# Optimization experiments

Hardware: AMD Instinct MI355X
Metric: run time of the kernel (lower is better)

Reference implementation:

```python
import jax, jax.numpy as jnp
import numpy as np

N = 100000  # nodes
E = 1600000  # edges
N_IN, N_H = 256, 128


def _norms(edge_src, edge_dst):
    ones = jnp.ones((E,), dtype=jnp.float32)
    out_deg = jax.ops.segment_sum(ones, edge_src, num_segments=N)
    in_deg = jax.ops.segment_sum(ones, edge_dst, num_segments=N)
    # DGL clamps degrees to >= 1 for norm='both'
    norm_src = jnp.clip(out_deg, 1.0, None) ** -0.5  # [N]
    norm_dst = jnp.clip(in_deg, 1.0, None) ** -0.5   # [N]
    return norm_src, norm_dst


def _graph_conv(h, W, b, edge_src, edge_dst, norm_src, norm_dst):
    # symmetric norm: D_out^{-1/2} A D_in^{-1/2}; W applied pre-aggregation
    h = h * norm_src[:, None]          # [N, d_in]
    h = h @ W                          # [N, d_out]
    msg = h[edge_src]                  # [E, d_out] gather
    agg = jax.ops.segment_sum(msg, edge_dst, num_segments=N)  # scatter-add
    agg = agg * norm_dst[:, None]
    return jax.nn.relu(agg + b)


def setup_inputs() -> dict:
    key = jax.random.key(0)
    ks = jax.random.split(key, 7)
    feat = jax.random.normal(ks[0], (1, N, N_IN), dtype=jnp.float32)
    edge_src = jax.random.randint(ks[1], (E,), 0, N, dtype=jnp.int32)
    edge_dst = jax.random.randint(ks[2], (E,), 0, N, dtype=jnp.int32)
    # Glorot-uniform weights as in DGL GraphConv reset_parameters
    lim1 = (6.0 / (N_IN + N_H)) ** 0.5
    lim2 = (6.0 / (N_H + N_H)) ** 0.5
    W1 = jax.random.uniform(ks[3], (N_IN, N_H), jnp.float32, -lim1, lim1)
    b1 = jnp.zeros((N_H,), dtype=jnp.float32)
    W2 = jax.random.uniform(ks[4], (N_H, N_H), jnp.float32, -lim2, lim2)
    b2 = jnp.zeros((N_H,), dtype=jnp.float32)
    return {"feat": feat, "W1": W1, "b1": b1, "W2": W2, "b2": b2,
            "edge_src": edge_src, "edge_dst": edge_dst}


def reference(feat, W1, b1, W2, b2, edge_src, edge_dst):
    h = feat.squeeze(0)  # [N, n_in]
    norm_src, norm_dst = _norms(edge_src, edge_dst)
    h = _graph_conv(h, W1, b1, edge_src, edge_dst, norm_src, norm_dst)
    h = _graph_conv(h, W2, b2, edge_src, edge_dst, norm_src, norm_dst)
    return h
```

## Files before the change

### kernel.cpp

```cpp
#include <hip/hip_runtime.h>
#include <hip/hip_bf16.h>

#define N_NODES 100000
#define N_EDGES 1600000
#define NBUCK 391
#define NBLK 256
#define CHUNK (N_EDGES / NBLK)
#define MATP (NBUCK * NBLK)

typedef float f32x4 __attribute__((ext_vector_type(4)));
typedef _Float16 f16x8 __attribute__((ext_vector_type(8)));

__device__ __forceinline__ void wt_elem(const float* __restrict__ W,
                                        _Float16* __restrict__ WTf,
                                        int K, int i) {
    int col = i / K, k = i - col * K;
    WTf[i] = (_Float16)W[(size_t)k * 128 + col];
}

__global__ __launch_bounds__(256) void fused_setup(
    const int* __restrict__ esrc, const int* __restrict__ edst,
    int* __restrict__ cnt_mat,
    const float* __restrict__ W1, _Float16* __restrict__ WT1f,
    const float* __restrict__ W2, _Float16* __restrict__ WT2f)
{
    __shared__ int hd[NBUCK], hs[NBUCK];
    const int b = blockIdx.x, t = threadIdx.x;
    if (b < NBLK) {
        for (int i = t; i < NBUCK; i += 256) { hd[i] = 0; hs[i] = 0; }
        __syncthreads();
        const int e1 = (b + 1) * CHUNK;
        for (int e = b * CHUNK + t; e < e1; e += 256) {
            atomicAdd(&hd[edst[e] >> 8], 1);
            atomicAdd(&hs[esrc[e] >> 8], 1);
        }
        __syncthreads();
        for (int i = t; i < NBUCK; i += 256) {
            cnt_mat[i * NBLK + b] = hd[i];
            cnt_mat[MATP + i * NBLK + b] = hs[i];
        }
    } else {
        int i = (b - NBLK) * 256 + t;
        if (i < 128 * 256) {
            wt_elem(W1, WT1f, 256, i);
        } else {
            int j = i - 128 * 256;
            wt_elem(W2, WT2f, 128, j);
        }
    }
}

__global__ __launch_bounds__(1024) void scan_blocks(const int* __restrict__ counts,
                                                    int* __restrict__ out,
                                                    int* __restrict__ partials, int n) {
    __shared__ int tmp[1024];
    int i = blockIdx.x * 1024 + threadIdx.x;
    int v = (i < n) ? counts[i] : 0;
    tmp[threadIdx.x] = v;
    __syncthreads();
    for (int off = 1; off < 1024; off <<= 1) {
        int t = (threadIdx.x >= (unsigned)off) ? tmp[threadIdx.x - off] : 0;
        __syncthreads();
        tmp[threadIdx.x] += t;
        __syncthreads();
    }
    if (i < n) out[i] = tmp[threadIdx.x] - v;
    if (threadIdx.x == 1023) partials[blockIdx.x] = tmp[1023];
}

__global__ __launch_bounds__(256) void scan_partials(int* __restrict__ partials, int nb) {
    __shared__ int tmp[256];
    int t = threadIdx.x;
    int v = (t < nb) ? partials[t] : 0;
    tmp[t] = v;
    __syncthreads();
    for (int off = 1; off < 256; off <<= 1) {
        int u = (t >= off) ? tmp[t - off] : 0;
        __syncthreads();
        tmp[t] += u;
        __syncthreads();
    }
    if (t < nb) partials[t] = tmp[t] - v;
}

__device__ __forceinline__ int sm_at(const int* __restrict__ scan_mat,
                                     const int* __restrict__ partials, int i) {
    return scan_mat[i] + partials[i >> 10];
}

__global__ __launch_bounds__(256) void bucket_scatter(const int* __restrict__ esrc,
                                                      const int* __restrict__ edst,
                                                      const int* __restrict__ scan_mat,
                                                      const int* __restrict__ partials,
                                                      unsigned int* __restrict__ tmp,
                                                      unsigned char* __restrict__ tmp2) {
    __shared__ int cd[NBUCK], cs[NBUCK];
    const int b = blockIdx.x, t = threadIdx.x;
    for (int i = t; i < NBUCK; i += 256) {
        cd[i] = sm_at(scan_mat, partials, i * NBLK + b);
        cs[i] = sm_at(scan_mat, partials, MATP + i * NBLK + b) - N_EDGES;
    }
    __syncthreads();
    const int e1 = (b + 1) * CHUNK;
    for (int e = b * CHUNK + t; e < e1; e += 256) {
        int s = esrc[e], d = edst[e];
        int pd = atomicAdd(&cd[d >> 8], 1);
        tmp[pd] = ((unsigned int)(d & 255) << 17) | (unsigned int)s;
        int ps = atomicAdd(&cs[s >> 8], 1);
        tmp2[ps] = (unsigned char)(s & 255);
    }
}

__global__ __launch_bounds__(256) void finalize_fused(
    const unsigned int* __restrict__ tmp,
    const unsigned char* __restrict__ tmp2,
    const int* __restrict__ scan_mat,
    const int* __restrict__ partials,
    int* __restrict__ rowptr,
    int* __restrict__ csr_src,
    float* __restrict__ ndst,
    float* __restrict__ nsrc)
{
    __shared__ int hist[256];
    __shared__ int scn[256];
    __shared__ int cur[256];
    const int bb = blockIdx.x, t = threadIdx.x;
    if (bb < NBUCK) {
        const int b = bb;
        const int beg = sm_at(scan_mat, partials, b * 256);
        const int end = sm_at(scan_mat, partials, (b + 1) * 256);
        hist[t] = 0;
        __syncthreads();
        for (int j = beg + t; j < end; j += 256)
            atomicAdd(&hist[tmp[j] >> 17], 1);
        __syncthreads();
        int v = hist[t];
        scn[t] = v;
        __syncthreads();
        for (int off = 1; off < 256; off <<= 1) {
            int u = (t >= off) ? scn[t - off] : 0;
            __syncthreads();
            scn[t] += u;
            __syncthreads();
        }
        int excl = scn[t] - v;
        int node = b * 256 + t;
        if (node <= N_NODES) rowptr[node] = beg + excl;
        if (node < N_NODES) ndst[node] = rsqrtf(fmaxf((float)v, 1.0f));
        cur[t] = beg + excl;
        __syncthreads();
        for (int j = beg + t; j < end; j += 256) {
            unsigned int x = tmp[j];
            int pos = atomicAdd(&cur[x >> 17], 1);
            csr_src[pos] = (int)(x & 0x1FFFFu);
        }
    } else {
        const int b = bb - NBUCK;
        const int beg = sm_at(scan_mat, partials, MATP + b * 256) - N_EDGES;
        const int end = (b < NBUCK - 1)
                          ? sm_at(scan_mat, partials, MATP + (b + 1) * 256) - N_EDGES
                          : N_EDGES;
        hist[t] = 0;
        __syncthreads();
        for (int j = beg + t; j < end; j += 256)
            atomicAdd(&hist[tmp2[j]], 1);
        __syncthreads();
        int node = b * 256 + t;
        if (node < N_NODES) nsrc[node] = rsqrtf(fmaxf((float)hist[t], 1.0f));
    }
}

template<int K, int ATERMS, typename AT>
__global__ __launch_bounds__(256) void gemm_mfma(
    const AT* __restrict__ A,
    const _Float16* __restrict__ WTf,
    const float* __restrict__ rowscale,
    _Float16* __restrict__ C16,
    int M)
{
    constexpr int ASTR = 520;
    constexpr int BSTR = 1032;
    __shared__ _Float16 Ah[8 * ASTR];
    __shared__ _Float16 Al[ATERMS == 2 ? 8 * ASTR : 8];
    __shared__ _Float16 Bf[8 * BSTR];

    const int tid = threadIdx.x;
    const int bm = blockIdx.x * 64;
    const int lane = tid & 63;
    const int wid = tid >> 6;
    const int wm = wid >> 1;
    const int wn = wid & 1;
    const int lr = lane & 15;
    const int lg = lane >> 4;

    f32x4 acc[2][4];
    #pragma unroll
    for (int i = 0; i < 2; ++i)
        #pragma unroll
        for (int j = 0; j < 4; ++j)
            acc[i][j] = (f32x4){0.f, 0.f, 0.f, 0.f};

    float avreg[2][8];
    f16x8 areg16[2];
    f16x8 bv[4];

    auto load_tile = [&](int k0) {
        #pragma unroll
        for (int i = 0; i < 2; ++i) {
            int lin = tid + i * 256;
            int row = lin >> 3;
            int s8  = lin & 7;
            int rg  = bm + row;
            if (rg < M) {
                const AT* ap = &A[(size_t)rg * K + k0 + s8 * 8];
                if constexpr (sizeof(AT) == 4) {
                    float4 v0 = *reinterpret_cast<const float4*>(ap);
                    float4 v1 = *reinterpret_cast<const float4*>(ap + 4);
                    avreg[i][0] = v0.x; avreg[i][1] = v0.y; avreg[i][2] = v0.z; avreg[i][3] = v0.w;
                    avreg[i][4] = v1.x; avreg[i][5] = v1.y; avreg[i][6] = v1.z; avreg[i][7] = v1.w;
                } else {
                    areg16[i] = *reinterpret_cast<const f16x8*>(ap);
                }
            } else {
                if constexpr (sizeof(AT) == 4) {
                    #pragma unroll
                    for (int j = 0; j < 8; ++j) avreg[i][j] = 0.f;
                } else {
                    #pragma unroll
                    for (int j = 0; j < 8; ++j) areg16[i][j] = (_Float16)0.f;
                }
            }
        }
        #pragma unroll
        for (int i = 0; i < 4; ++i) {
            int lin = tid + i * 256;
            int col = lin >> 3;
            int s8  = lin & 7;
            bv[i] = *reinterpret_cast<const f16x8*>(&WTf[(size_t)col * K + k0 + s8 * 8]);
        }
    };

    load_tile(0);

    for (int k0 = 0; k0 < K; k0 += 64) {
        {
            #pragma unroll
            for (int i = 0; i < 2; ++i) {
                int lin = tid + i * 256;
                int row = lin >> 3;
                int s8  = lin & 7;
                int off = s8 * ASTR + row * 8;
                if constexpr (sizeof(AT) == 4) {
                    f16x8 vh, vl;
                    #pragma unroll
                    for (int j = 0; j < 8; ++j) {
                        _Float16 h = (_Float16)avreg[i][j];
                        vh[j] = h;
                        vl[j] = (_Float16)(avreg[i][j] - (float)h);
                    }
                    *reinterpret_cast<f16x8*>(&Ah[off]) = vh;
                    if constexpr (ATERMS == 2)
                        *reinterpret_cast<f16x8*>(&Al[off]) = vl;
                } else {
                    *reinterpret_cast<f16x8*>(&Ah[off]) = areg16[i];
                }
            }
            #pragma unroll
            for (int i = 0; i < 4; ++i) {
                int lin = tid + i * 256;
                int col = lin >> 3;
                int s8  = lin & 7;
                *reinterpret_cast<f16x8*>(&Bf[s8 * BSTR + col * 8]) = bv[i];
            }
        }
        __syncthreads();

        if (k0 + 64 < K) load_tile(k0 + 64);

        #pragma unroll
        for (int ks = 0; ks < 2; ++ks) {
            const int slot = ks * 4 + lg;
            f16x8 afh[2], afl[2], bf[4];
            #pragma unroll
            for (int mt = 0; mt < 2; ++mt) {
                int row = wm * 32 + mt * 16 + lr;
                int off = slot * ASTR + row * 8;
                afh[mt] = *reinterpret_cast<const f16x8*>(&Ah[off]);
                if constexpr (ATERMS == 2)
                    afl[mt] = *reinterpret_cast<const f16x8*>(&Al[off]);
            }
            #pragma unroll
            for (int nt = 0; nt < 4; ++nt) {
                int col = wn * 64 + nt * 16 + lr;
                bf[nt] = *reinterpret_cast<const f16x8*>(&Bf[slot * BSTR + col * 8]);
            }
            #pragma unroll
            for (int mt = 0; mt < 2; ++mt) {
                #pragma unroll
                for (int nt = 0; nt < 4; ++nt) {
                    acc[mt][nt] = __builtin_amdgcn_mfma_f32_16x16x32_f16(
                        afh[mt], bf[nt], acc[mt][nt], 0, 0, 0);
                    if constexpr (ATERMS == 2)
                        acc[mt][nt] = __builtin_amdgcn_mfma_f32_16x16x32_f16(
                            afl[mt], bf[nt], acc[mt][nt], 0, 0, 0);
                }
            }
        }
        __syncthreads();
    }

    #pragma unroll
    for (int mt = 0; mt < 2; ++mt) {
        #pragma unroll
        for (int r = 0; r < 4; ++r) {
            int row = bm + wm * 32 + mt * 16 + lg * 4 + r;
            if (row < M) {
                float s = rowscale[row];
                #pragma unroll
                for (int nt = 0; nt < 4; ++nt) {
                    int col = wn * 64 + nt * 16 + lr;
                    C16[(size_t)row * 128 + col] = (_Float16)(acc[mt][nt][r] * s);
                }
            }
        }
    }
}

template<typename OT>
__global__ __launch_bounds__(256) void aggregate16(
    const _Float16* __restrict__ h16,
    const int* __restrict__ rowptr,
    const int* __restrict__ csr_src,
    const float* __restrict__ ndst,
    const float* __restrict__ bias,
    OT* __restrict__ out, int N)
{
    int g = blockIdx.x * blockDim.x + threadIdx.x;
    int node = g >> 4;
    if (node >= N) return;
    int c8 = (g & 15) * 8;
    int beg = rowptr[node];
    int end = rowptr[node + 1];
    float acc[8] = {0.f, 0.f, 0.f, 0.f, 0.f, 0.f, 0.f, 0.f};
    int j = beg;
    for (; j + 3 < end; j += 4) {
        int s0 = csr_src[j];
        int s1 = csr_src[j + 1];
        int s2 = csr_src[j + 2];
        int s3 = csr_src[j + 3];
        f16x8 v0 = *reinterpret_cast<const f16x8*>(&h16[(size_t)s0 * 128 + c8]);
        f16x8 v1 = *reinterpret_cast<const f16x8*>(&h16[(size_t)s1 * 128 + c8]);
        f16x8 v2 = *reinterpret_cast<const f16x8*>(&h16[(size_t)s2 * 128 + c8]);
        f16x8 v3 = *reinterpret_cast<const f16x8*>(&h16[(size_t)s3 * 128 + c8]);
        #pragma unroll
        for (int k = 0; k < 8; ++k)
            acc[k] += ((float)v0[k] + (float)v1[k]) + ((float)v2[k] + (float)v3[k]);
    }
    for (; j < end; ++j) {
        int s0 = csr_src[j];
        f16x8 v0 = *reinterpret_cast<const f16x8*>(&h16[(size_t)s0 * 128 + c8]);
        #pragma unroll
        for (int k = 0; k < 8; ++k) acc[k] += (float)v0[k];
    }
    float sc = ndst[node];
    const float4 b0 = *reinterpret_cast<const float4*>(&bias[c8]);
    const float4 b1 = *reinterpret_cast<const float4*>(&bias[c8 + 4]);
    float r[8];
    r[0] = fmaxf(acc[0] * sc + b0.x, 0.f);
    r[1] = fmaxf(acc[1] * sc + b0.y, 0.f);
    r[2] = fmaxf(acc[2] * sc + b0.z, 0.f);
    r[3] = fmaxf(acc[3] * sc + b0.w, 0.f);
    r[4] = fmaxf(acc[4] * sc + b1.x, 0.f);
    r[5] = fmaxf(acc[5] * sc + b1.y, 0.f);
    r[6] = fmaxf(acc[6] * sc + b1.z, 0.f);
    r[7] = fmaxf(acc[7] * sc + b1.w, 0.f);
    OT* op = &out[(size_t)node * 128 + c8];
    if constexpr (sizeof(OT) == 4) {
        float4 r0 = {r[0], r[1], r[2], r[3]};
        float4 r1 = {r[4], r[5], r[6], r[7]};
        *reinterpret_cast<float4*>(op) = r0;
        *reinterpret_cast<float4*>(op + 4) = r1;
    } else {
        f16x8 rv;
        #pragma unroll
        for (int k = 0; k < 8; ++k) rv[k] = (_Float16)r[k];
        *reinterpret_cast<f16x8*>(op) = rv;
    }
}

extern "C" void kernel_launch(void* const* d_in, const int* in_sizes, int n_in,
                              void* d_out, int out_size, void* d_ws, size_t ws_size,
                              hipStream_t stream) {
    const float* feat = (const float*)d_in[0];
    const float* W1   = (const float*)d_in[1];
    const float* b1   = (const float*)d_in[2];
    const float* W2   = (const float*)d_in[3];
    const float* b2   = (const float*)d_in[4];
    const int* esrc   = (const int*)d_in[5];
    const int* edst   = (const int*)d_in[6];
    float* out = (float*)d_out;

    const int Nn = N_NODES, E = N_EDGES;
    const int SCAN_N = 2 * MATP;
    const int SCAN_NB = (SCAN_N + 1023) / 1024;

    float* hseg   = (float*)d_ws;
    _Float16* h16   = (_Float16*)hseg;
    _Float16* h1out = h16 + (size_t)Nn * 128;
    _Float16* WT1f = (_Float16*)(hseg + (size_t)Nn * 128);
    _Float16* WT2f = WT1f + 128 * 256;
    int* csr_src  = (int*)(WT2f + 128 * 128);
    int* rowptr   = csr_src + E;
    unsigned int* tmp = (unsigned int*)(rowptr + 100004);
    unsigned char* tmp2 = (unsigned char*)(tmp + (size_t)E);
    int* cnt_mat  = (int*)(tmp2 + (((size_t)E + 15) & ~15ull));
    int* scan_mat = cnt_mat + SCAN_N;
    int* partials = scan_mat + SCAN_N;
    float* nsrc   = (float*)(partials + ((SCAN_NB + 3) & ~3));
    float* ndst   = nsrc + Nn;

    fused_setup<<<NBLK + 192, 256, 0, stream>>>(esrc, edst, cnt_mat, W1, WT1f, W2, WT2f);

    scan_blocks<<<SCAN_NB, 1024, 0, stream>>>(cnt_mat, scan_mat, partials, SCAN_N);
    scan_partials<<<1, 256, 0, stream>>>(partials, SCAN_NB);

    bucket_scatter<<<NBLK, 256, 0, stream>>>(esrc, edst, scan_mat, partials, tmp, tmp2);
    finalize_fused<<<2 * NBUCK, 256, 0, stream>>>(tmp, tmp2, scan_mat, partials,
                                                  rowptr, csr_src, ndst, nsrc);

    const int gemm_grid = (Nn + 63) / 64;
    const int agg_grid  = (Nn * 16 + 255) / 256;

    gemm_mfma<256, 2, float><<<gemm_grid, 256, 0, stream>>>(feat, WT1f, nsrc, h16, Nn);
    aggregate16<_Float16><<<agg_grid, 256, 0, stream>>>(
        h16, rowptr, csr_src, ndst, b1, h1out, Nn);

    gemm_mfma<128, 1, _Float16><<<gemm_grid, 256, 0, stream>>>(h1out, WT2f, nsrc, h16, Nn);
    aggregate16<float><<<agg_grid, 256, 0, stream>>>(
        h16, rowptr, csr_src, ndst, b2, out, Nn);
}
```

Baseline: 225.3 us.

## Overlap layer-1 GEMM with CSR build by co-launching in heterogeneous kernels

Result: faster. 219.8 us (-2.5%).

```diff
diff --git a/kernel.cpp b/kernel.cpp
--- a/kernel.cpp
+++ b/kernel.cpp
@@ -7,6 +7,9 @@
 #define NBLK 256
 #define CHUNK (N_EDGES / NBLK)
 #define MATP (NBUCK * NBLK)
+#define GEMM_GRID 1563
+#define GA 782
+#define GB (GEMM_GRID - GA)
 
 typedef float f32x4 __attribute__((ext_vector_type(4)));
 typedef _Float16 f16x8 __attribute__((ext_vector_type(8)));
@@ -88,104 +91,20 @@
     return scan_mat[i] + partials[i >> 10];
 }
 
-__global__ __launch_bounds__(256) void bucket_scatter(const int* __restrict__ esrc,
-                                                      const int* __restrict__ edst,
-                                                      const int* __restrict__ scan_mat,
-                                                      const int* __restrict__ partials,
-                                                      unsigned int* __restrict__ tmp,
-                                                      unsigned char* __restrict__ tmp2) {
-    __shared__ int cd[NBUCK], cs[NBUCK];
-    const int b = blockIdx.x, t = threadIdx.x;
-    for (int i = t; i < NBUCK; i += 256) {
-        cd[i] = sm_at(scan_mat, partials, i * NBLK + b);
-        cs[i] = sm_at(scan_mat, partials, MATP + i * NBLK + b) - N_EDGES;
-    }
-    __syncthreads();
-    const int e1 = (b + 1) * CHUNK;
-    for (int e = b * CHUNK + t; e < e1; e += 256) {
-        int s = esrc[e], d = edst[e];
-        int pd = atomicAdd(&cd[d >> 8], 1);
-        tmp[pd] = ((unsigned int)(d & 255) << 17) | (unsigned int)s;
-        int ps = atomicAdd(&cs[s >> 8], 1);
-        tmp2[ps] = (unsigned char)(s & 255);
-    }
-}
-
-__global__ __launch_bounds__(256) void finalize_fused(
-    const unsigned int* __restrict__ tmp,
-    const unsigned char* __restrict__ tmp2,
-    const int* __restrict__ scan_mat,
-    const int* __restrict__ partials,
-    int* __restrict__ rowptr,
-    int* __restrict__ csr_src,
-    float* __restrict__ ndst,
-    float* __restrict__ nsrc)
-{
-    __shared__ int hist[256];
-    __shared__ int scn[256];
-    __shared__ int cur[256];
-    const int bb = blockIdx.x, t = threadIdx.x;
-    if (bb < NBUCK) {
-        const int b = bb;
-        const int beg = sm_at(scan_mat, partials, b * 256);
-        const int end = sm_at(scan_mat, partials, (b + 1) * 256);
-        hist[t] = 0;
-        __syncthreads();
-        for (int j = beg + t; j < end; j += 256)
-            atomicAdd(&hist[tmp[j] >> 17], 1);
-        __syncthreads();
-        int v = hist[t];
-        scn[t] = v;
-        __syncthreads();
-        for (int off = 1; off < 256; off <<= 1) {
-            int u = (t >= off) ? scn[t - off] : 0;
-            __syncthreads();
-            scn[t] += u;
-            __syncthreads();
-        }
-        int excl = scn[t] - v;
-        int node = b * 256 + t;
-        if (node <= N_NODES) rowptr[node] = beg + excl;
-        if (node < N_NODES) ndst[node] = rsqrtf(fmaxf((float)v, 1.0f));
-        cur[t] = beg + excl;
-        __syncthreads();
-        for (int j = beg + t; j < end; j += 256) {
-            unsigned int x = tmp[j];
-            int pos = atomicAdd(&cur[x >> 17], 1);
-            csr_src[pos] = (int)(x & 0x1FFFFu);
-        }
-    } else {
-        const int b = bb - NBUCK;
-        const int beg = sm_at(scan_mat, partials, MATP + b * 256) - N_EDGES;
-        const int end = (b < NBUCK - 1)
-                          ? sm_at(scan_mat, partials, MATP + (b + 1) * 256) - N_EDGES
-                          : N_EDGES;
-        hist[t] = 0;
-        __syncthreads();
-        for (int j = beg + t; j < end; j += 256)
-            atomicAdd(&hist[tmp2[j]], 1);
-        __syncthreads();
-        int node = b * 256 + t;
-        if (node < N_NODES) nsrc[node] = rsqrtf(fmaxf((float)hist[t], 1.0f));
-    }
-}
-
-template<int K, int ATERMS, typename AT>
-__global__ __launch_bounds__(256) void gemm_mfma(
-    const AT* __restrict__ A,
-    const _Float16* __restrict__ WTf,
-    const float* __restrict__ rowscale,
-    _Float16* __restrict__ C16,
-    int M)
+template<int K, int ATERMS, bool SCALE, typename AT>
+__device__ __forceinline__ void gemm_body(
+    char* __restrict__ smem_raw, int gblk,
+    const AT* __restrict__ A, const _Float16* __restrict__ WTf,
+    const float* __restrict__ rowscale, _Float16* __restrict__ C16, int M)
 {
     constexpr int ASTR = 520;
     constexpr int BSTR = 1032;
-    __shared__ _Float16 Ah[8 * ASTR];
-    __shared__ _Float16 Al[ATERMS == 2 ? 8 * ASTR : 8];
-    __shared__ _Float16 Bf[8 * BSTR];
+    _Float16* Ah = (_Float16*)smem_raw;
+    _Float16* Al = Ah + 8 * ASTR;
+    _Float16* Bf = (ATERMS == 2) ? (Al + 8 * ASTR) : Al;
 
     const int tid = threadIdx.x;
-    const int bm = blockIdx.x * 64;
+    const int bm = gblk * 64;
     const int lane = tid & 63;
     const int wid = tid >> 6;
     const int wm = wid >> 1;
@@ -315,7 +234,7 @@
         for (int r = 0; r < 4; ++r) {
             int row = bm + wm * 32 + mt * 16 + lg * 4 + r;
             if (row < M) {
-                float s = rowscale[row];
+                float s = SCALE ? rowscale[row] : 1.0f;
                 #pragma unroll
                 for (int nt = 0; nt < 4; ++nt) {
                     int col = wn * 64 + nt * 16 + lr;
@@ -326,11 +245,132 @@
     }
 }
 
-template<typename OT>
+__device__ __forceinline__ void scatter_body(
+    char* __restrict__ smem_raw, int b,
+    const int* __restrict__ esrc, const int* __restrict__ edst,
+    const int* __restrict__ scan_mat, const int* __restrict__ partials,
+    unsigned int* __restrict__ tmp, unsigned char* __restrict__ tmp2)
+{
+    int* cd = (int*)smem_raw;
+    int* cs = cd + NBUCK;
+    const int t = threadIdx.x;
+    for (int i = t; i < NBUCK; i += 256) {
+        cd[i] = sm_at(scan_mat, partials, i * NBLK + b);
+        cs[i] = sm_at(scan_mat, partials, MATP + i * NBLK + b) - N_EDGES;
+    }
+    __syncthreads();
+    const int e1 = (b + 1) * CHUNK;
+    for (int e = b * CHUNK + t; e < e1; e += 256) {
+        int s = esrc[e], d = edst[e];
+        int pd = atomicAdd(&cd[d >> 8], 1);
+        tmp[pd] = ((unsigned int)(d & 255) << 17) | (unsigned int)s;
+        int ps = atomicAdd(&cs[s >> 8], 1);
+        tmp2[ps] = (unsigned char)(s & 255);
+    }
+}
+
+__device__ __forceinline__ void finalize_body(
+    char* __restrict__ smem_raw, int bb,
+    const unsigned int* __restrict__ tmp, const unsigned char* __restrict__ tmp2,
+    const int* __restrict__ scan_mat, const int* __restrict__ partials,
+    int* __restrict__ rowptr, int* __restrict__ csr_src,
+    float* __restrict__ ndst, float* __restrict__ nsrc)
+{
+    int* hist = (int*)smem_raw;
+    int* scn  = hist + 256;
+    int* cur  = scn + 256;
+    const int t = threadIdx.x;
+    if (bb < NBUCK) {
+        const int b = bb;
+        const int beg = sm_at(scan_mat, partials, b * 256);
+        const int end = sm_at(scan_mat, partials, (b + 1) * 256);
+        hist[t] = 0;
+        __syncthreads();
+        for (int j = beg + t; j < end; j += 256)
+            atomicAdd(&hist[tmp[j] >> 17], 1);
+        __syncthreads();
+        int v = hist[t];
+        scn[t] = v;
+        __syncthreads();
+        for (int off = 1; off < 256; off <<= 1) {
+            int u = (t >= off) ? scn[t - off] : 0;
+            __syncthreads();
+            scn[t] += u;
+            __syncthreads();
+        }
+        int excl = scn[t] - v;
+        int node = b * 256 + t;
+        if (node <= N_NODES) rowptr[node] = beg + excl;
+        if (node < N_NODES) ndst[node] = rsqrtf(fmaxf((float)v, 1.0f));
+        cur[t] = beg + excl;
+        __syncthreads();
+        for (int j = beg + t; j < end; j += 256) {
+            unsigned int x = tmp[j];
+            int pos = atomicAdd(&cur[x >> 17], 1);
+            csr_src[pos] = (int)(x & 0x1FFFFu);
+        }
+    } else {
+        const int b = bb - NBUCK;
+        const int beg = sm_at(scan_mat, partials, MATP + b * 256) - N_EDGES;
+        const int end = (b < NBUCK - 1)
+                          ? sm_at(scan_mat, partials, MATP + (b + 1) * 256) - N_EDGES
+                          : N_EDGES;
+        hist[t] = 0;
+        __syncthreads();
+        for (int j = beg + t; j < end; j += 256)
+            atomicAdd(&hist[tmp2[j]], 1);
+        __syncthreads();
+        int node = b * 256 + t;
+        if (node < N_NODES) nsrc[node] = rsqrtf(fmaxf((float)hist[t], 1.0f));
+    }
+}
+
+__global__ __launch_bounds__(256) void scatter_gemmA(
+    const int* __restrict__ esrc, const int* __restrict__ edst,
+    const int* __restrict__ scan_mat, const int* __restrict__ partials,
+    unsigned int* __restrict__ tmp, unsigned char* __restrict__ tmp2,
+    const float* __restrict__ feat, const _Float16* __restrict__ WT1f,
+    _Float16* __restrict__ h16, int N)
+{
+    __shared__ __align__(16) char smem[33152];
+    if (blockIdx.x < NBLK)
+        scatter_body(smem, blockIdx.x, esrc, edst, scan_mat, partials, tmp, tmp2);
+    else
+        gemm_body<256, 2, false, float>(smem, blockIdx.x - NBLK, feat, WT1f,
+                                        nullptr, h16, N);
+}
+
+__global__ __launch_bounds__(256) void finalize_gemmB(
+    const unsigned int* __restrict__ tmp, const unsigned char* __restrict__ tmp2,
+    const int* __restrict__ scan_mat, const int* __restrict__ partials,
+    int* __restrict__ rowptr, int* __restrict__ csr_src,
+    float* __restrict__ ndst, float* __restrict__ nsrc,
+    const float* __restrict__ feat, const _Float16* __restrict__ WT1f,
+    _Float16* __restrict__ h16, int N)
+{
+    __shared__ __align__(16) char smem[33152];
+    if (blockIdx.x < 2 * NBUCK)
+        finalize_body(smem, blockIdx.x, tmp, tmp2, scan_mat, partials,
+                      rowptr, csr_src, ndst, nsrc);
+    else
+        gemm_body<256, 2, false, float>(smem, GA + (blockIdx.x - 2 * NBUCK),
+                                        feat, WT1f, nullptr, h16, N);
+}
+
+__global__ __launch_bounds__(256) void gemm2_kernel(
+    const _Float16* __restrict__ A, const _Float16* __restrict__ WTf,
+    const float* __restrict__ rowscale, _Float16* __restrict__ C16, int M)
+{
+    __shared__ __align__(16) char smem[24832];
+    gemm_body<128, 1, true, _Float16>(smem, blockIdx.x, A, WTf, rowscale, C16, M);
+}
+
+template<typename OT, bool SRCSCALE>
 __global__ __launch_bounds__(256) void aggregate16(
     const _Float16* __restrict__ h16,
     const int* __restrict__ rowptr,
     const int* __restrict__ csr_src,
+    const float* __restrict__ nsrc,
     const float* __restrict__ ndst,
     const float* __restrict__ bias,
     OT* __restrict__ out, int N)
@@ -352,15 +392,29 @@
         f16x8 v1 = *reinterpret_cast<const f16x8*>(&h16[(size_t)s1 * 128 + c8]);
         f16x8 v2 = *reinterpret_cast<const f16x8*>(&h16[(size_t)s2 * 128 + c8]);
         f16x8 v3 = *reinterpret_cast<const f16x8*>(&h16[(size_t)s3 * 128 + c8]);
-        #pragma unroll
-        for (int k = 0; k < 8; ++k)
-            acc[k] += ((float)v0[k] + (float)v1[k]) + ((float)v2[k] + (float)v3[k]);
+        if constexpr (SRCSCALE) {
+            float n0 = nsrc[s0], n1 = nsrc[s1], n2 = nsrc[s2], n3 = nsrc[s3];
+            #pragma unroll
+            for (int k = 0; k < 8; ++k)
+                acc[k] += ((float)v0[k] * n0 + (float)v1[k] * n1)
+                        + ((float)v2[k] * n2 + (float)v3[k] * n3);
+        } else {
+            #pragma unroll
+            for (int k = 0; k < 8; ++k)
+                acc[k] += ((float)v0[k] + (float)v1[k]) + ((float)v2[k] + (float)v3[k]);
+        }
     }
     for (; j < end; ++j) {
         int s0 = csr_src[j];
         f16x8 v0 = *reinterpret_cast<const f16x8*>(&h16[(size_t)s0 * 128 + c8]);
-        #pragma unroll
-        for (int k = 0; k < 8; ++k) acc[k] += (float)v0[k];
+        if constexpr (SRCSCALE) {
+            float n0 = nsrc[s0];
+            #pragma unroll
+            for (int k = 0; k < 8; ++k) acc[k] += (float)v0[k] * n0;
+        } else {
+            #pragma unroll
+            for (int k = 0; k < 8; ++k) acc[k] += (float)v0[k];
+        }
     }
     float sc = ndst[node];
     const float4 b0 = *reinterpret_cast<const float4*>(&bias[c8]);
@@ -424,18 +478,19 @@
     scan_blocks<<<SCAN_NB, 1024, 0, stream>>>(cnt_mat, scan_mat, partials, SCAN_N);
     scan_partials<<<1, 256, 0, stream>>>(partials, SCAN_NB);
 
-    bucket_scatter<<<NBLK, 256, 0, stream>>>(esrc, edst, scan_mat, partials, tmp, tmp2);
-    finalize_fused<<<2 * NBUCK, 256, 0, stream>>>(tmp, tmp2, scan_mat, partials,
-                                                  rowptr, csr_src, ndst, nsrc);
-
-    const int gemm_grid = (Nn + 63) / 64;
-    const int agg_grid  = (Nn * 16 + 255) / 256;
-
-    gemm_mfma<256, 2, float><<<gemm_grid, 256, 0, stream>>>(feat, WT1f, nsrc, h16, Nn);
-    aggregate16<_Float16><<<agg_grid, 256, 0, stream>>>(
-        h16, rowptr, csr_src, ndst, b1, h1out, Nn);
-
-    gemm_mfma<128, 1, _Float16><<<gemm_grid, 256, 0, stream>>>(h1out, WT2f, nsrc, h16, Nn);
-    aggregate16<float><<<agg_grid, 256, 0, stream>>>(
-        h16, rowptr, csr_src, ndst, b2, out, Nn);
-}
+    scatter_gemmA<<<NBLK + GA, 256, 0, stream>>>(esrc, edst, scan_mat, partials,
+                                                 tmp, tmp2, feat, WT1f, h16, Nn);
+    finalize_gemmB<<<2 * NBUCK + GB, 256, 0, stream>>>(tmp, tmp2, scan_mat, partials,
+                                                       rowptr, csr_src, ndst, nsrc,
+                                                       feat, WT1f, h16, Nn);
+
+    const int agg_grid = (Nn * 16 + 255) / 256;
+
+    aggregate16<_Float16, true><<<agg_grid, 256, 0, stream>>>(
+        h16, rowptr, csr_src, nsrc, ndst, b1, h1out, Nn);
+
+    gemm2_kernel<<<GEMM_GRID, 256, 0, stream>>>(h1out, WT2f, nsrc, h16, Nn);
+
+    aggregate16<float, false><<<agg_grid, 256, 0, stream>>>(
+        h16, rowptr, csr_src, nsrc, ndst, b2, out, Nn);
+}
```
